# Kernel tuning notes

Measured on AMD Instinct MI355X. Metric: run time of the kernel, lower is better.

The kernel has to match this reference:

```python
import jax, jax.numpy as jnp
import numpy as np

D_MODEL = 2048
D_HEAD = 128
NUM_HEADS = 16
D_LATENT = 512
B, S = 4, 2048


def setup_inputs() -> dict:
    key = jax.random.key(0)
    ks = jax.random.split(key, 11)
    sc = lambda fan_in: 1.0 / np.sqrt(fan_in)
    x = jax.random.normal(ks[0], (B, S, D_MODEL), dtype=jnp.float32)
    # weights stored as [in, out] (transpose of torch nn.Linear.weight)
    W_down = jax.random.uniform(ks[1], (D_MODEL, D_LATENT), jnp.float32, -sc(D_MODEL), sc(D_MODEL))
    b_down = jax.random.uniform(ks[2], (D_LATENT,), jnp.float32, -sc(D_MODEL), sc(D_MODEL))
    W_uk = jax.random.uniform(ks[3], (D_LATENT, D_MODEL), jnp.float32, -sc(D_LATENT), sc(D_LATENT))
    b_uk = jax.random.uniform(ks[4], (D_MODEL,), jnp.float32, -sc(D_LATENT), sc(D_LATENT))
    W_uv = jax.random.uniform(ks[5], (D_LATENT, D_MODEL), jnp.float32, -sc(D_LATENT), sc(D_LATENT))
    b_uv = jax.random.uniform(ks[6], (D_MODEL,), jnp.float32, -sc(D_LATENT), sc(D_LATENT))
    W_q = jax.random.uniform(ks[7], (D_MODEL, NUM_HEADS * D_HEAD), jnp.float32, -sc(D_MODEL), sc(D_MODEL))
    b_q = jax.random.uniform(ks[8], (NUM_HEADS * D_HEAD,), jnp.float32, -sc(D_MODEL), sc(D_MODEL))
    W_o = jax.random.uniform(ks[9], (NUM_HEADS * D_HEAD, D_MODEL), jnp.float32, -sc(NUM_HEADS * D_HEAD), sc(NUM_HEADS * D_HEAD))
    b_o = jax.random.uniform(ks[10], (D_MODEL,), jnp.float32, -sc(NUM_HEADS * D_HEAD), sc(NUM_HEADS * D_HEAD))
    return {"x": x, "W_down": W_down, "b_down": b_down, "W_uk": W_uk, "b_uk": b_uk,
            "W_uv": W_uv, "b_uv": b_uv, "W_q": W_q, "b_q": b_q, "W_o": W_o, "b_o": b_o}


def reference(x, W_down, b_down, W_uk, b_uk, W_uv, b_uv, W_q, b_q, W_o, b_o):
    b, s, _ = x.shape
    latents = x @ W_down + b_down                      # [B,S,L]
    keys = latents @ W_uk + b_uk                       # [B,S,D]
    values = latents @ W_uv + b_uv                     # [B,S,D]
    q = (x @ W_q + b_q).reshape(b, s, NUM_HEADS, D_HEAD).transpose(0, 2, 1, 3)
    k = keys.reshape(b, s, NUM_HEADS, D_HEAD).transpose(0, 2, 1, 3)
    v = values.reshape(b, s, NUM_HEADS, D_HEAD).transpose(0, 2, 1, 3)
    scores = jnp.einsum('bhqd,bhkd->bhqk', q, k) / np.sqrt(D_HEAD).astype(np.float32)
    attn = jax.nn.softmax(scores, axis=-1)
    ctx = jnp.einsum('bhqk,bhkd->bhqd', attn, v)       # [B,H,S,Dh]
    ctx = ctx.transpose(0, 2, 1, 3).reshape(b, s, NUM_HEADS * D_HEAD)
    return ctx @ W_o + b_o
```

## Files before the change

kernel.cpp:

```cpp
#include <hip/hip_runtime.h>

#define D_MODEL 2048
#define D_LATENT 512
#define NUM_HEADS 16
#define D_HEAD 128
#define BATCH 4
#define SEQ 2048
#define MTOK (BATCH*SEQ)

typedef __bf16 bf16_t;
typedef __bf16 bf16x4 __attribute__((ext_vector_type(4)));
typedef __bf16 bf16x8 __attribute__((ext_vector_type(8)));
typedef float  f32x4  __attribute__((ext_vector_type(4)));

__device__ __forceinline__ void load_lds16(const bf16_t* g, bf16_t* l) {
  __builtin_amdgcn_global_load_lds(
      (const __attribute__((address_space(1))) void*)g,
      (__attribute__((address_space(3))) void*)l,
      16, 0, 0);
}

__global__ void convert_f32_bf16_kernel(const float* __restrict__ src,
                                        bf16_t* __restrict__ dst, int n4) {
  int i = blockIdx.x * 256 + threadIdx.x;
  if (i >= n4) return;
  float4 v = *(const float4*)&src[(size_t)i * 4];
  bf16x4 o = { (bf16_t)v.x, (bf16_t)v.y, (bf16_t)v.z, (bf16_t)v.w };
  *(bf16x4*)&dst[(size_t)i * 4] = o;
}

__global__ void transpose_w_kernel(const float* __restrict__ src, bf16_t* __restrict__ dst,
                                   int R, int C) {
  __shared__ __align__(16) bf16_t tile[64][66];
  int rt = blockIdx.y * 64, ct = blockIdx.x * 64;
  int lc = threadIdx.x & 63, lr = threadIdx.x >> 6;
  for (int i = 0; i < 64; i += 4)
    tile[lr + i][lc] = (bf16_t)src[(size_t)(rt + lr + i) * C + ct + lc];
  __syncthreads();
  for (int i = 0; i < 64; i += 4)
    dst[(size_t)(ct + lr + i) * R + rt + lc] = tile[lc][lr + i];
}

__global__ void transpose_v_kernel(const bf16_t* __restrict__ v, bf16_t* __restrict__ vt) {
  __shared__ __align__(16) bf16_t tile[64][66];
  int bh = blockIdx.z; int b = bh >> 4, h = bh & 15;
  int st = blockIdx.x * 64, dt = blockIdx.y * 64;
  int lc = threadIdx.x & 63, lr = threadIdx.x >> 6;
  const bf16_t* src = v + (size_t)b * SEQ * D_MODEL + h * D_HEAD;
  for (int i = 0; i < 64; i += 4)
    tile[lr + i][lc] = src[(size_t)(st + lr + i) * D_MODEL + dt + lc];
  __syncthreads();
  bf16_t* dst = vt + (size_t)bh * D_HEAD * SEQ;
  for (int i = 0; i < 64; i += 4)
    dst[(size_t)(dt + lr + i) * SEQ + st + lc] = tile[lc][lr + i];
}

template<typename OutT>
__global__ __launch_bounds__(256, 2) void gemm_bt_kernel(
    const bf16_t* __restrict__ A, const bf16_t* __restrict__ Wt,
    const float* __restrict__ bias, OutT* __restrict__ C,
    int M, int N, int K, float premul)
{
  __shared__ __align__(16) bf16_t As[128 * 32];
  __shared__ __align__(16) bf16_t Bs[128 * 32];
  int tid = threadIdx.x;
  int lane = tid & 63, wave = tid >> 6;
  int wr = (wave >> 1) * 64, wc = (wave & 1) * 64;
  size_t row0 = (size_t)blockIdx.x * 128, col0 = (size_t)blockIdx.y * 128;
  int lr = lane & 15, quad = lane >> 4, rq = quad * 4;

  f32x4 acc[4][4] = {};

  int srow = wave * 32 + (lane >> 2);
  int scol = ((lane & 3) ^ ((lane >> 3) & 3)) * 8;
  const bf16_t* Ag = A  + (row0 + srow) * K + scol;
  const bf16_t* Bg = Wt + (col0 + srow) * K + scol;
  bf16_t* Asw = As + wave * 1024;
  bf16_t* Bsw = Bs + wave * 1024;

  int rchunk = (quad ^ ((lr >> 1) & 3)) * 8;

  for (int k0 = 0; k0 < K; k0 += 32) {
    __syncthreads();
    load_lds16(Ag,          Asw);
    load_lds16(Ag + 16 * K, Asw + 512);
    load_lds16(Bg,          Bsw);
    load_lds16(Bg + 16 * K, Bsw + 512);
    Ag += 32; Bg += 32;
    __syncthreads();

    bf16x8 af[4], bfr[4];
    #pragma unroll
    for (int mi = 0; mi < 4; ++mi)
      af[mi] = *(const bf16x8*)&As[(wr + mi * 16 + lr) * 32 + rchunk];
    #pragma unroll
    for (int ni = 0; ni < 4; ++ni)
      bfr[ni] = *(const bf16x8*)&Bs[(wc + ni * 16 + lr) * 32 + rchunk];
    #pragma unroll
    for (int mi = 0; mi < 4; ++mi)
      #pragma unroll
      for (int ni = 0; ni < 4; ++ni)
        acc[mi][ni] = __builtin_amdgcn_mfma_f32_16x16x32_bf16(af[mi], bfr[ni], acc[mi][ni], 0, 0, 0);
  }

  #pragma unroll
  for (int ni = 0; ni < 4; ++ni) {
    int col = (int)col0 + wc + ni * 16 + lr;
    float bv = bias[col];
    #pragma unroll
    for (int mi = 0; mi < 4; ++mi) {
      #pragma unroll
      for (int r = 0; r < 4; ++r) {
        size_t row = row0 + wr + mi * 16 + rq + r;
        C[row * N + col] = (OutT)((acc[mi][ni][r] + bv) * premul);
      }
    }
  }
}

__global__ __launch_bounds__(256, 2) void attention_kernel(
    const bf16_t* __restrict__ q, const bf16_t* __restrict__ keys,
    const bf16_t* __restrict__ vt, bf16_t* __restrict__ ctx)
{
  __shared__ __align__(16) bf16_t KP[128 * 72];
  __shared__ __align__(16) bf16_t Vs[128][72];
  bf16_t (*Ks)[136] = (bf16_t (*)[136])KP;
  bf16_t (*Ps)[72]  = (bf16_t (*)[72])KP;
  int bh = blockIdx.y; int b = bh >> 4, h = bh & 15;
  int qt = blockIdx.x;
  int tid = threadIdx.x, lane = tid & 63, wave = tid >> 6;
  int lr = lane & 15, quad = lane >> 4, kq = quad * 8, rq = quad * 4;

  const bf16_t* qg = q    + (size_t)(b * SEQ + qt * 128) * D_MODEL + h * D_HEAD;
  const bf16_t* kg = keys + (size_t)b * SEQ * D_MODEL + h * D_HEAD;
  const bf16_t* vg = vt   + (size_t)bh * D_HEAD * SEQ;

  bf16x8 qf[2][4];
  #pragma unroll
  for (int mi = 0; mi < 2; ++mi)
    #pragma unroll
    for (int ks = 0; ks < 4; ++ks)
      qf[mi][ks] = *(const bf16x8*)&qg[(size_t)(wave*32 + mi*16 + lr) * D_MODEL + ks*32 + kq];

  bf16x8 kreg[4], vreg[4];
  const bf16_t* kp4[4];
  const bf16_t* vp4[4];
  bf16_t* kd4[4];
  bf16_t* vd4[4];
  #pragma unroll
  for (int i = 0; i < 4; ++i) {
    int c = tid + i * 256;
    int r = c >> 4, kc = (c & 15) * 8;
    kp4[i] = kg + (size_t)r * D_MODEL + kc;
    kd4[i] = &Ks[r][kc];
    int d = c >> 3, vc = (c & 7) * 8;
    vp4[i] = vg + (size_t)d * SEQ + vc;
    vd4[i] = &Vs[d][vc];
  }
  #pragma unroll
  for (int i = 0; i < 4; ++i) {
    kreg[i] = *(const bf16x8*)kp4[i];
    vreg[i] = *(const bf16x8*)vp4[i];
  }

  f32x4 accO[2][8] = {};
  float m2[2]   = {-1e30f, -1e30f};
  float lsum[2] = {0.f, 0.f};

  for (int kt = 0; kt < SEQ/64; ++kt) {
    __syncthreads();
    #pragma unroll
    for (int i = 0; i < 4; ++i) {
      *(bf16x8*)kd4[i] = kreg[i];
      *(bf16x8*)vd4[i] = vreg[i];
    }
    __syncthreads();

    f32x4 sc[2][4] = {};
    #pragma unroll
    for (int ks = 0; ks < 4; ++ks) {
      bf16x8 kf[4];
      #pragma unroll
      for (int ni = 0; ni < 4; ++ni) kf[ni] = *(const bf16x8*)&Ks[ni*16 + lr][ks*32 + kq];
      __builtin_amdgcn_s_setprio(1);
      #pragma unroll
      for (int mi = 0; mi < 2; ++mi)
        #pragma unroll
        for (int ni = 0; ni < 4; ++ni)
          sc[mi][ni] = __builtin_amdgcn_mfma_f32_16x16x32_bf16(kf[ni], qf[mi][ks], sc[mi][ni], 0, 0, 0);
      __builtin_amdgcn_s_setprio(0);
    }

    __syncthreads();

    if (kt + 1 < SEQ/64) {
      #pragma unroll
      for (int i = 0; i < 4; ++i) {
        kp4[i] += 64 * D_MODEL;
        vp4[i] += 64;
        kreg[i] = *(const bf16x8*)kp4[i];
        vreg[i] = *(const bf16x8*)vp4[i];
      }
    }

    #pragma unroll
    for (int mi = 0; mi < 2; ++mi) {
      float rm = sc[mi][0][0];
      #pragma unroll
      for (int ni = 0; ni < 4; ++ni)
        #pragma unroll
        for (int r = 0; r < 4; ++r) rm = fmaxf(rm, sc[mi][ni][r]);
      rm = fmaxf(rm, __shfl_xor(rm, 16, 64));
      rm = fmaxf(rm, __shfl_xor(rm, 32, 64));

      if (!__all(rm - m2[mi] <= 8.0f)) {
        float mnew  = fmaxf(m2[mi], rm);
        float alpha = exp2f(m2[mi] - mnew);
        m2[mi] = mnew;
        lsum[mi] *= alpha;
        float ar[4];
        #pragma unroll
        for (int r = 0; r < 4; ++r) ar[r] = __shfl(alpha, rq + r, 16);
        #pragma unroll
        for (int nd = 0; nd < 8; ++nd)
          #pragma unroll
          for (int r = 0; r < 4; ++r) accO[mi][nd][r] *= ar[r];
      }

      float rs = 0.f;
      int prow = wave*32 + mi*16 + lr;
      #pragma unroll
      for (int ni = 0; ni < 4; ++ni) {
        float p0 = exp2f(sc[mi][ni][0] - m2[mi]);
        float p1 = exp2f(sc[mi][ni][1] - m2[mi]);
        float p2 = exp2f(sc[mi][ni][2] - m2[mi]);
        float p3 = exp2f(sc[mi][ni][3] - m2[mi]);
        rs += (p0 + p1) + (p2 + p3);
        bf16x4 pk = { (bf16_t)p0, (bf16_t)p1, (bf16_t)p2, (bf16_t)p3 };
        *(bf16x4*)&Ps[prow][ni*16 + rq] = pk;
      }
      rs += __shfl_xor(rs, 16, 64);
      rs += __shfl_xor(rs, 32, 64);
      lsum[mi] += rs;
    }


    #pragma unroll
    for (int ks2 = 0; ks2 < 2; ++ks2) {
      bf16x8 pf[2], vf[8];
      #pragma unroll
      for (int mi = 0; mi < 2; ++mi)
        pf[mi] = *(const bf16x8*)&Ps[wave*32 + mi*16 + lr][ks2*32 + kq];
      #pragma unroll
      for (int nd = 0; nd < 8; ++nd)
        vf[nd] = *(const bf16x8*)&Vs[nd*16 + lr][ks2*32 + kq];
      __builtin_amdgcn_s_setprio(1);
      #pragma unroll
      for (int mi = 0; mi < 2; ++mi)
        #pragma unroll
        for (int nd = 0; nd < 8; ++nd)
          accO[mi][nd] = __builtin_amdgcn_mfma_f32_16x16x32_bf16(pf[mi], vf[nd], accO[mi][nd], 0, 0, 0);
      __builtin_amdgcn_s_setprio(0);
    }
  }

  bf16_t* og = ctx + (size_t)(b * SEQ + qt * 128) * D_MODEL + h * D_HEAD;
  #pragma unroll
  for (int mi = 0; mi < 2; ++mi) {
    float inv[4];
    #pragma unroll
    for (int r = 0; r < 4; ++r) inv[r] = 1.0f / __shfl(lsum[mi], rq + r, 16);
    #pragma unroll
    for (int r = 0; r < 4; ++r) {
      int row = wave*32 + mi*16 + rq + r;
      #pragma unroll
      for (int nd = 0; nd < 8; ++nd)
        og[(size_t)row * D_MODEL + nd*16 + lr] = (bf16_t)(accO[mi][nd][r] * inv[r]);
    }
  }
}

extern "C" void kernel_launch(void* const* d_in, const int* in_sizes, int n_in,
                              void* d_out, int out_size, void* d_ws, size_t ws_size,
                              hipStream_t stream) {
  const float* x      = (const float*)d_in[0];
  const float* W_down = (const float*)d_in[1];
  const float* b_down = (const float*)d_in[2];
  const float* W_uk   = (const float*)d_in[3];
  const float* b_uk   = (const float*)d_in[4];
  const float* W_uv   = (const float*)d_in[5];
  const float* b_uv   = (const float*)d_in[6];
  const float* W_q    = (const float*)d_in[7];
  const float* b_q    = (const float*)d_in[8];
  const float* W_o    = (const float*)d_in[9];
  const float* b_o    = (const float*)d_in[10];
  float* out = (float*)d_out;

  char* ws = (char*)d_ws;
  bf16_t* xb      = (bf16_t*)ws;  ws += (size_t)MTOK*D_MODEL*2;
  bf16_t* Wt_down = (bf16_t*)ws;  ws += (size_t)D_LATENT*D_MODEL*2;
  bf16_t* Wt_uk   = (bf16_t*)ws;  ws += (size_t)D_MODEL*D_LATENT*2;
  bf16_t* Wt_uv   = (bf16_t*)ws;  ws += (size_t)D_MODEL*D_LATENT*2;
  bf16_t* Wt_q    = (bf16_t*)ws;  ws += (size_t)D_MODEL*D_MODEL*2;
  bf16_t* Wt_o    = (bf16_t*)ws;  ws += (size_t)D_MODEL*D_MODEL*2;
  bf16_t* lat     = (bf16_t*)ws;  ws += (size_t)MTOK*D_LATENT*2;
  bf16_t* keys    = (bf16_t*)ws;  ws += (size_t)MTOK*D_MODEL*2;
  bf16_t* vals    = (bf16_t*)ws;  ws += (size_t)MTOK*D_MODEL*2;
  bf16_t* qm      = (bf16_t*)ws;  ws += (size_t)MTOK*D_MODEL*2;
  bf16_t* vtm     = (bf16_t*)ws;  ws += (size_t)MTOK*D_MODEL*2;
  bf16_t* ctx     = vals;

  const float cs = 0.0883883476483184f * 1.44269504089f;

  convert_f32_bf16_kernel<<<(MTOK*D_MODEL/4 + 255)/256, 256, 0, stream>>>(x, xb, MTOK*D_MODEL/4);

  transpose_w_kernel<<<dim3(D_LATENT/64, D_MODEL/64), 256, 0, stream>>>(W_down, Wt_down, D_MODEL, D_LATENT);
  transpose_w_kernel<<<dim3(D_MODEL/64, D_LATENT/64), 256, 0, stream>>>(W_uk,   Wt_uk,   D_LATENT, D_MODEL);
  transpose_w_kernel<<<dim3(D_MODEL/64, D_LATENT/64), 256, 0, stream>>>(W_uv,   Wt_uv,   D_LATENT, D_MODEL);
  transpose_w_kernel<<<dim3(D_MODEL/64, D_MODEL/64),  256, 0, stream>>>(W_q,    Wt_q,    D_MODEL,  D_MODEL);
  transpose_w_kernel<<<dim3(D_MODEL/64, D_MODEL/64),  256, 0, stream>>>(W_o,    Wt_o,    D_MODEL,  D_MODEL);

  gemm_bt_kernel<bf16_t><<<dim3(MTOK/128, D_LATENT/128), 256, 0, stream>>>(xb,  Wt_down, b_down, lat,  MTOK, D_LATENT, D_MODEL, 1.0f);
  gemm_bt_kernel<bf16_t><<<dim3(MTOK/128, D_MODEL/128),  256, 0, stream>>>(lat, Wt_uk,   b_uk,   keys, MTOK, D_MODEL,  D_LATENT, 1.0f);
  gemm_bt_kernel<bf16_t><<<dim3(MTOK/128, D_MODEL/128),  256, 0, stream>>>(lat, Wt_uv,   b_uv,   vals, MTOK, D_MODEL,  D_LATENT, 1.0f);
  gemm_bt_kernel<bf16_t><<<dim3(MTOK/128, D_MODEL/128),  256, 0, stream>>>(xb,  Wt_q,    b_q,    qm,   MTOK, D_MODEL,  D_MODEL, cs);

  transpose_v_kernel<<<dim3(SEQ/64, D_HEAD/64, BATCH*NUM_HEADS), 256, 0, stream>>>(vals, vtm);

  attention_kernel<<<dim3(SEQ/128, BATCH*NUM_HEADS), 256, 0, stream>>>(qm, keys, vtm, ctx);

  gemm_bt_kernel<float><<<dim3(MTOK/128, D_MODEL/128), 256, 0, stream>>>(ctx, Wt_o, b_o, out, MTOK, D_MODEL, D_MODEL, 1.0f);
}
```

Baseline: 613.0 us.

## Add 256x256 eight-wave pipelined GEMM kernel for the large projections

Adds a new GEMM kernel with 256x256 output tiles, 8 waves, a 4-slot LDS ring buffer fed by direct global-to-LDS loads, XOR-swizzled LDS layout and a workgroup swizzle for L2 locality. The loads of later K stages are interleaved with MFMA sub-blocks under barriers and priority hints. It replaces the 128x128 GEMM for the key, value, query and output projections, aiming for more data reuse per tile and better overlap of memory traffic with compute. In exchange it has higher register and LDS pressure and fewer workgroups per launch.

```diff
diff --git a/kernel.cpp b/kernel.cpp
--- a/kernel.cpp
+++ b/kernel.cpp
@@ -118,6 +118,157 @@
   }
 }
 
+template<typename OutT, int K>
+__global__ __launch_bounds__(512, 2) void gemm8_kernel(
+    const bf16_t* __restrict__ A, const bf16_t* __restrict__ Wt,
+    const float* __restrict__ bias, OutT* __restrict__ C,
+    int M, int N, float premul)
+{
+  constexpr int NT = K / 64;
+  __shared__ __align__(16) bf16_t AS[4 * 8192];
+  __shared__ __align__(16) bf16_t BS[4 * 8192];
+  int tid = threadIdx.x, lane = tid & 63, wave = tid >> 6;
+  int wm = wave >> 2, wn = wave & 3;
+  int lr = lane & 15, quad = lane >> 4, rq = quad * 4;
+  int rsw = lr & 7;
+
+  int mtiles = M >> 8;
+  int nwg = gridDim.x;
+  int wg = blockIdx.x;
+  int swz = (wg & 7) * (nwg >> 3) + (wg >> 3);
+  size_t row0 = (size_t)(swz % mtiles) * 256;
+  size_t col0 = (size_t)(swz / mtiles) * 256;
+
+  int srow = (wave << 3) + (lane >> 3);
+  int scol = ((lane & 7) ^ (lane >> 3)) * 8;
+  const bf16_t* Abase = A  + (row0 + srow) * K + scol;
+  const bf16_t* Bbase = Wt + (col0 + srow) * K + scol;
+
+  auto stageA = [&](int j) {
+    int kt = j >> 1, half = j & 1, slot = j & 3;
+    const bf16_t* g = Abase + (size_t)(half * 128) * K + kt * 64;
+    bf16_t* l = AS + slot * 8192 + wave * 512;
+    load_lds16(g,                l);
+    load_lds16(g + (size_t)64 * K, l + 4096);
+  };
+  auto stageB = [&](int j) {
+    int kt = j >> 1, half = j & 1, slot = j & 3;
+    const bf16_t* g = Bbase + (size_t)(half * 128) * K + kt * 64;
+    bf16_t* l = BS + slot * 8192 + wave * 512;
+    load_lds16(g,                l);
+    load_lds16(g + (size_t)64 * K, l + 4096);
+  };
+
+  f32x4 acc[8][4] = {};
+  bf16x8 aF[4][2], bF[2][2][2];
+
+  stageA(0); stageB(0); stageA(1); stageB(1); stageA(2); stageB(2);
+  asm volatile("s_waitcnt vmcnt(4)" ::: "memory");
+  __builtin_amdgcn_s_barrier();
+
+  for (int s = 0; s < NT; ++s) {
+    const bf16_t* Asl = AS + ((2 * s + wm) & 3) * 8192;
+    const bf16_t* Bsl = BS + ((2 * s + (wn >> 1)) & 3) * 8192;
+
+    #pragma unroll
+    for (int m = 0; m < 4; ++m)
+      #pragma unroll
+      for (int kh = 0; kh < 2; ++kh)
+        aF[m][kh] = *(const bf16x8*)&Asl[(m * 16 + lr) * 64 + (((kh * 4 + quad) ^ rsw) * 8)];
+    #pragma unroll
+    for (int n = 0; n < 2; ++n)
+      #pragma unroll
+      for (int kh = 0; kh < 2; ++kh)
+        bF[0][n][kh] = *(const bf16x8*)&Bsl[((wn & 1) * 64 + n * 16 + lr) * 64 + (((kh * 4 + quad) ^ rsw) * 8)];
+    if (2 * s + 3 < 2 * NT) stageA(2 * s + 3);
+    __builtin_amdgcn_s_barrier();
+    asm volatile("s_waitcnt lgkmcnt(0)" ::: "memory");
+    __builtin_amdgcn_sched_barrier(0);
+    __builtin_amdgcn_s_setprio(1);
+    #pragma unroll
+    for (int m = 0; m < 4; ++m)
+      #pragma unroll
+      for (int n = 0; n < 2; ++n)
+        #pragma unroll
+        for (int kh = 0; kh < 2; ++kh)
+          acc[m][n] = __builtin_amdgcn_mfma_f32_16x16x32_bf16(aF[m][kh], bF[0][n][kh], acc[m][n], 0, 0, 0);
+    __builtin_amdgcn_s_setprio(0);
+    __builtin_amdgcn_s_barrier();
+
+    #pragma unroll
+    for (int n = 0; n < 2; ++n)
+      #pragma unroll
+      for (int kh = 0; kh < 2; ++kh)
+        bF[1][n][kh] = *(const bf16x8*)&Bsl[((wn & 1) * 64 + 32 + n * 16 + lr) * 64 + (((kh * 4 + quad) ^ rsw) * 8)];
+    if (2 * s + 3 < 2 * NT) stageB(2 * s + 3);
+    __builtin_amdgcn_s_barrier();
+    asm volatile("s_waitcnt lgkmcnt(0)" ::: "memory");
+    __builtin_amdgcn_sched_barrier(0);
+    __builtin_amdgcn_s_setprio(1);
+    #pragma unroll
+    for (int m = 0; m < 4; ++m)
+      #pragma unroll
+      for (int n = 0; n < 2; ++n)
+        #pragma unroll
+        for (int kh = 0; kh < 2; ++kh)
+          acc[m][2 + n] = __builtin_amdgcn_mfma_f32_16x16x32_bf16(aF[m][kh], bF[1][n][kh], acc[m][2 + n], 0, 0, 0);
+    __builtin_amdgcn_s_setprio(0);
+    __builtin_amdgcn_s_barrier();
+
+    #pragma unroll
+    for (int m = 0; m < 4; ++m)
+      #pragma unroll
+      for (int kh = 0; kh < 2; ++kh)
+        aF[m][kh] = *(const bf16x8*)&Asl[(64 + m * 16 + lr) * 64 + (((kh * 4 + quad) ^ rsw) * 8)];
+    if (2 * s + 4 < 2 * NT) stageB(2 * s + 4);
+    __builtin_amdgcn_s_barrier();
+    asm volatile("s_waitcnt lgkmcnt(0)" ::: "memory");
+    __builtin_amdgcn_sched_barrier(0);
+    __builtin_amdgcn_s_setprio(1);
+    #pragma unroll
+    for (int m = 0; m < 4; ++m)
+      #pragma unroll
+      for (int n = 0; n < 2; ++n)
+        #pragma unroll
+        for (int kh = 0; kh < 2; ++kh)
+          acc[4 + m][n] = __builtin_amdgcn_mfma_f32_16x16x32_bf16(aF[m][kh], bF[0][n][kh], acc[4 + m][n], 0, 0, 0);
+    __builtin_amdgcn_s_setprio(0);
+    __builtin_amdgcn_s_barrier();
+
+    if (2 * s + 4 < 2 * NT) stageA(2 * s + 4);
+    __builtin_amdgcn_s_barrier();
+    __builtin_amdgcn_s_setprio(1);
+    #pragma unroll
+    for (int m = 0; m < 4; ++m)
+      #pragma unroll
+      for (int n = 0; n < 2; ++n)
+        #pragma unroll
+        for (int kh = 0; kh < 2; ++kh)
+          acc[4 + m][2 + n] = __builtin_amdgcn_mfma_f32_16x16x32_bf16(aF[m][kh], bF[1][n][kh], acc[4 + m][2 + n], 0, 0, 0);
+    __builtin_amdgcn_s_setprio(0);
+    if (s < NT - 2)       asm volatile("s_waitcnt vmcnt(4)" ::: "memory");
+    else if (s == NT - 2) asm volatile("s_waitcnt vmcnt(0)" ::: "memory");
+    __builtin_amdgcn_s_barrier();
+  }
+
+  #pragma unroll
+  for (int mh = 0; mh < 2; ++mh)
+    #pragma unroll
+    for (int nh = 0; nh < 2; ++nh)
+      #pragma unroll
+      for (int n = 0; n < 2; ++n) {
+        int col = (int)col0 + wn * 64 + nh * 32 + n * 16 + lr;
+        float bv = bias[col];
+        #pragma unroll
+        for (int m = 0; m < 4; ++m)
+          #pragma unroll
+          for (int r = 0; r < 4; ++r) {
+            size_t row = row0 + wm * 128 + mh * 64 + m * 16 + rq + r;
+            C[row * N + col] = (OutT)((acc[mh * 4 + m][nh * 2 + n][r] + bv) * premul);
+          }
+      }
+}
+
 __global__ __launch_bounds__(256, 2) void attention_kernel(
     const bf16_t* __restrict__ q, const bf16_t* __restrict__ keys,
     const bf16_t* __restrict__ vt, bf16_t* __restrict__ ctx)
@@ -243,7 +394,6 @@
       rs += __shfl_xor(rs, 32, 64);
       lsum[mi] += rs;
     }
-
 
     #pragma unroll
     for (int ks2 = 0; ks2 < 2; ++ks2) {
@@ -321,13 +471,14 @@
   transpose_w_kernel<<<dim3(D_MODEL/64, D_MODEL/64),  256, 0, stream>>>(W_o,    Wt_o,    D_MODEL,  D_MODEL);
 
   gemm_bt_kernel<bf16_t><<<dim3(MTOK/128, D_LATENT/128), 256, 0, stream>>>(xb,  Wt_down, b_down, lat,  MTOK, D_LATENT, D_MODEL, 1.0f);
-  gemm_bt_kernel<bf16_t><<<dim3(MTOK/128, D_MODEL/128),  256, 0, stream>>>(lat, Wt_uk,   b_uk,   keys, MTOK, D_MODEL,  D_LATENT, 1.0f);
-  gemm_bt_kernel<bf16_t><<<dim3(MTOK/128, D_MODEL/128),  256, 0, stream>>>(lat, Wt_uv,   b_uv,   vals, MTOK, D_MODEL,  D_LATENT, 1.0f);
-  gemm_bt_kernel<bf16_t><<<dim3(MTOK/128, D_MODEL/128),  256, 0, stream>>>(xb,  Wt_q,    b_q,    qm,   MTOK, D_MODEL,  D_MODEL, cs);
+
+  gemm8_kernel<bf16_t, 512><<<(MTOK/256)*(D_MODEL/256), 512, 0, stream>>>(lat, Wt_uk, b_uk, keys, MTOK, D_MODEL, 1.0f);
+  gemm8_kernel<bf16_t, 512><<<(MTOK/256)*(D_MODEL/256), 512, 0, stream>>>(lat, Wt_uv, b_uv, vals, MTOK, D_MODEL, 1.0f);
+  gemm8_kernel<bf16_t, 2048><<<(MTOK/256)*(D_MODEL/256), 512, 0, stream>>>(xb, Wt_q, b_q, qm, MTOK, D_MODEL, cs);
 
   transpose_v_kernel<<<dim3(SEQ/64, D_HEAD/64, BATCH*NUM_HEADS), 256, 0, stream>>>(vals, vtm);
 
   attention_kernel<<<dim3(SEQ/128, BATCH*NUM_HEADS), 256, 0, stream>>>(qm, keys, vtm, ctx);
 
-  gemm_bt_kernel<float><<<dim3(MTOK/128, D_MODEL/128), 256, 0, stream>>>(ctx, Wt_o, b_o, out, MTOK, D_MODEL, D_MODEL, 1.0f);
-}
+  gemm8_kernel<float, 2048><<<(MTOK/256)*(D_MODEL/256), 512, 0, stream>>>(ctx, Wt_o, b_o, out, MTOK, D_MODEL, 1.0f);
+}
```

Result: slower. 643.1 us (+4.9%).
